# Kernel tuning notes

Hardware: AMD Instinct MI355X
Metric: run time of the kernel (lower is better)

The kernel has to match this reference:

```python
import jax, jax.numpy as jnp
import numpy as np

N, K = 65536, 4
X_SIZE, H_SIZE = 300, 256


def setup_inputs() -> dict:
    key = jax.random.key(0)
    ks = jax.random.split(key, 11)
    s = 0.05  # small init scale for weights
    return {
        "x": jax.random.normal(ks[0], (N, X_SIZE), jnp.float32),
        "h_msgs": jax.random.normal(ks[1], (N, K, H_SIZE), jnp.float32),
        "c_msgs": jax.random.normal(ks[2], (N, K, H_SIZE), jnp.float32),
        "W_iou": jax.random.normal(ks[3], (3 * H_SIZE, X_SIZE), jnp.float32) * s,
        "b_iou": jax.random.normal(ks[4], (3 * H_SIZE,), jnp.float32) * s,
        "U_iou": jax.random.normal(ks[5], (3 * H_SIZE, H_SIZE), jnp.float32) * s,
        "b_Uiou": jax.random.normal(ks[6], (3 * H_SIZE,), jnp.float32) * s,
        "W_f": jax.random.normal(ks[7], (H_SIZE, X_SIZE), jnp.float32) * s,
        "b_Wf": jax.random.normal(ks[8], (H_SIZE,), jnp.float32) * s,
        "U_f": jax.random.normal(ks[9], (H_SIZE, H_SIZE), jnp.float32) * s,
        "b_Uf": jax.random.normal(ks[10], (H_SIZE,), jnp.float32) * s,
    }


def reference(x, h_msgs, c_msgs, W_iou, b_iou, U_iou, b_Uiou, W_f, b_Wf, U_f, b_Uf):
    # ----- reduce_func: gather children states, gated forget sum -----
    h_tild = jnp.sum(h_msgs, axis=1)                              # [N, H]
    wx = (x @ W_f.T + b_Wf)[:, None, :]                           # [N, 1, H]
    uh = jnp.einsum('nkh,gh->nkg', h_msgs, U_f) + b_Uf            # [N, K, H]
    f = jax.nn.sigmoid(wx + uh)                                   # [N, K, H]
    c_tild = jnp.sum(f * c_msgs, axis=1)                          # [N, H]

    # ----- apply_func: fused i/o/u gates -----
    iou = (x @ W_iou.T + b_iou) + (h_tild @ U_iou.T + b_Uiou)     # [N, 3H]
    i, o, u = jnp.split(iou, 3, axis=1)
    i, o, u = jax.nn.sigmoid(i), jax.nn.sigmoid(o), jnp.tanh(u)
    c = i * u + c_tild
    h = o * jnp.tanh(c)
    return jnp.stack((h, c))                                      # [2, N, H]
```

## Files before the change

kernel.cpp:

```cpp
#include <hip/hip_runtime.h>


typedef __attribute__((ext_vector_type(8))) short short8;
typedef __attribute__((ext_vector_type(4))) float f32x4;
typedef __attribute__((ext_vector_type(4))) unsigned short us4;
typedef __attribute__((ext_vector_type(4))) unsigned int u32x4;

#define NN 65536

__device__ __forceinline__ unsigned short f2bf(float f) {
  unsigned int u = __float_as_uint(f);
  u += 0x7FFFu + ((u >> 16) & 1u);
  return (unsigned short)(u >> 16);
}
__device__ __forceinline__ float bf2f(unsigned short s) {
  return __uint_as_float(((unsigned int)s) << 16);
}
__device__ __forceinline__ f32x4 mfma16(short8 a, short8 b, f32x4 c) {
  return __builtin_amdgcn_mfma_f32_16x16x32_bf16(a, b, c, 0, 0, 0);
}
__device__ __forceinline__ float sigmoidf_(float v) { return 1.0f / (1.0f + __expf(-v)); }
__device__ __forceinline__ float ftanh(float v) { return 1.0f - 2.0f / (__expf(2.0f * v) + 1.0f); }

__global__ void prep_all(const float* __restrict__ Wf, const float* __restrict__ Uf,
                         const float* __restrict__ Wiou, const float* __restrict__ Uiou,
                         unsigned short* __restrict__ ws) {
  int idx = blockIdx.x * 256 + threadIdx.x;
  if (idx < 81920) {
    int j = idx & 7, lane = (idx >> 3) & 63, ct = (idx >> 9) & 15, kt = idx >> 13;
    int k = kt*32 + ((lane >> 4) << 3) + j, col = ct*16 + (lane & 15);
    ws[idx] = f2bf(k < 300 ? Wf[col*300 + k] : 0.0f);
  } else if (idx < 147456) {
    int i = idx - 81920;
    int j = i & 7, lane = (i >> 3) & 63, ct = (i >> 9) & 15, kt = i >> 13;
    int k = kt*32 + ((lane >> 4) << 3) + j, col = ct*16 + (lane & 15);
    ws[idx] = f2bf(Uf[col*256 + k]);
  } else {
    int i = idx - 147456;
    int j = i & 7, lane = (i >> 3) & 63;
    int rest = i >> 9, ct = rest % 48, kt = rest / 48;
    int k = kt*32 + ((lane >> 4) << 3) + j;
    int g = (ct % 3)*256 + (ct/3)*16 + (lane & 15);
    float v = (k < 320) ? (k < 300 ? Wiou[g*300 + k] : 0.0f) : Uiou[g*256 + (k - 320)];
    ws[idx] = f2bf(v);
  }
}

__global__ __launch_bounds__(512, 4) void fused_cell(
    const float* __restrict__ x, const float* __restrict__ h_msgs,
    const float* __restrict__ c_msgs,
    const float* __restrict__ b_iou, const float* __restrict__ b_Uiou,
    const float* __restrict__ bWf, const float* __restrict__ bUf,
    const unsigned short* __restrict__ Bwf, const unsigned short* __restrict__ Buf,
    const unsigned short* __restrict__ Biou,
    float* __restrict__ out_h, float* __restrict__ out_c) {
  __shared__ alignas(16) char smem[71168];
  unsigned short* Axh = (unsigned short*)smem;
  unsigned short* Hm  = (unsigned short*)(smem + 37376);
  unsigned short* wfs = (unsigned short*)(smem + 54272);
  unsigned int*   IUO = (unsigned int*)(smem + 37376);

  const int tid = threadIdx.x;
  const int n0 = blockIdx.x * 32;
  const int wave = tid >> 6, lane = tid & 63;
  const int lrow = lane & 15, lgrp = lane >> 4;
  const int nl = wave;
  const f32x4 fz = {0.0f, 0.0f, 0.0f, 0.0f};

  f32x4 hvN[4];

  auto issue_h = [&](int chunk) {
    int node = n0 + chunk*8 + nl;
    const float* hp = h_msgs + (size_t)node*1024 + lane*4;
#pragma unroll
    for (int k = 0; k < 4; ++k) hvN[k] = *(const f32x4*)(hp + k*256);
  };

  auto write_h = [&](int chunk) {
    f32x4 s = fz;
#pragma unroll
    for (int k = 0; k < 4; ++k) {
      us4 o;
#pragma unroll
      for (int e = 0; e < 4; ++e) { s[e] += hvN[k][e]; o[e] = f2bf(hvN[k][e]); }
      *(us4*)&Hm[(nl*4 + k)*264 + lane*4] = o;
    }
    us4 ht;
#pragma unroll
    for (int e = 0; e < 4; ++e) ht[e] = f2bf(s[e]);
    *(us4*)&Axh[(chunk*8 + nl)*584 + 320 + lane*4] = ht;
  };

  auto uh_gemm = [&](f32x4 a2[2][2]) {
    const unsigned short* bp = Buf + ((wave*2)*64 + lane)*8;
    short8 b0 = *(const short8*)bp;
    short8 b1 = *(const short8*)(bp + 512);
#pragma unroll
    for (int ks = 0; ks < 8; ++ks) {
      short8 nb0 = b0, nb1 = b1;
      if (ks < 7) {
        const unsigned short* np = Buf + (((ks+1)*16 + wave*2)*64 + lane)*8;
        nb0 = *(const short8*)np;
        nb1 = *(const short8*)(np + 512);
      }
#pragma unroll
      for (int rt = 0; rt < 2; ++rt) {
        short8 a = *(const short8*)&Hm[(rt*16 + lrow)*264 + ks*32 + lgrp*8];
        a2[rt][0] = mfma16(a, b0, a2[rt][0]);
        a2[rt][1] = mfma16(a, b1, a2[rt][1]);
      }
      b0 = nb0; b1 = nb1;
    }
  };

  issue_h(0);
  for (int i = tid; i < 32*80; i += 512) {
    int r = i / 80, c4 = i - r*80;
    f32x4 v = fz;
    if (c4 < 75) v = *(const f32x4*)&x[(size_t)(n0 + r)*300 + c4*4];
    us4 o;
#pragma unroll
    for (int e = 0; e < 4; ++e) o[e] = f2bf(v[e]);
    *(us4*)&Axh[r*584 + c4*4] = o;
  }
  write_h(0);
  issue_h(1);
  __syncthreads();

  {
    const unsigned short* bp = Bwf + ((wave*2)*64 + lane)*8;
    short8 b0 = *(const short8*)bp;
    short8 b1 = *(const short8*)(bp + 512);
    f32x4 w00 = fz, w01 = fz, w10 = fz, w11 = fz;
#pragma unroll
    for (int ks = 0; ks < 10; ++ks) {
      short8 nb0 = b0, nb1 = b1;
      if (ks < 9) {
        const unsigned short* np = Bwf + (((ks+1)*16 + wave*2)*64 + lane)*8;
        nb0 = *(const short8*)np;
        nb1 = *(const short8*)(np + 512);
      }
      short8 a0 = *(const short8*)&Axh[lrow*584 + ks*32 + lgrp*8];
      short8 a1 = *(const short8*)&Axh[(16 + lrow)*584 + ks*32 + lgrp*8];
      w00 = mfma16(a0, b0, w00); w10 = mfma16(a1, b0, w10);
      w01 = mfma16(a0, b1, w01); w11 = mfma16(a1, b1, w11);
      b0 = nb0; b1 = nb1;
    }
#pragma unroll
    for (int ct = 0; ct < 2; ++ct) {
      int col = wave*32 + ct*16 + lrow;
      float bias = bWf[col];
      f32x4 v0 = ct ? w01 : w00, v1 = ct ? w11 : w10;
#pragma unroll
      for (int r = 0; r < 4; ++r) {
        wfs[(lgrp*4 + r)*264 + col]      = f2bf(v0[r] + bias);
        wfs[(16 + lgrp*4 + r)*264 + col] = f2bf(v1[r] + bias);
      }
    }
  }
  __syncthreads();

  float bu[2];
  bu[0] = bUf[wave*32 + lrow];
  bu[1] = bUf[wave*32 + 16 + lrow];

#pragma unroll
  for (int chunk = 0; chunk < 4; ++chunk) {
    float cm[2][2][4];
#pragma unroll
    for (int rt = 0; rt < 2; ++rt) {
      const float* cp = c_msgs + (size_t)(n0 + chunk*8 + rt*4 + lgrp)*1024 + wave*32 + lrow;
#pragma unroll
      for (int ct2 = 0; ct2 < 2; ++ct2)
#pragma unroll
        for (int r = 0; r < 4; ++r) cm[rt][ct2][r] = cp[r*256 + ct2*16];
    }

    f32x4 a2[2][2] = {{fz, fz}, {fz, fz}};
    uh_gemm(a2);

#pragma unroll
    for (int rt = 0; rt < 2; ++rt) {
      int node = chunk*8 + rt*4 + lgrp;
#pragma unroll
      for (int ct2 = 0; ct2 < 2; ++ct2) {
        int col = wave*32 + ct2*16 + lrow;
        float wfv = bf2f(wfs[node*264 + col]);
        float s = 0.0f;
#pragma unroll
        for (int r = 0; r < 4; ++r) {
          float fg = sigmoidf_(a2[rt][ct2][r] + wfv + bu[ct2]);
          s += fg * cm[rt][ct2][r];
        }
        out_c[(size_t)(n0 + node)*256 + col] = s;
      }
    }
    __syncthreads();
    if (chunk < 3) {
      write_h(chunk + 1);
      if (chunk < 2) issue_h(chunk + 2);
      __syncthreads();
    }
  }

#pragma unroll 1
  for (int p = 0; p < 2; ++p) {
    int cb = wave*2 + p;
    int ct0 = cb*3;
    int col = cb*16 + lrow;
    f32x4 aI0 = fz, aO0 = fz, aU0 = fz, aI1 = fz, aO1 = fz, aU1 = fz;
    const unsigned short* bp = Biou + ((size_t)ct0*64 + lane)*8;
    short8 bi = *(const short8*)bp;
    short8 bo = *(const short8*)(bp + 512);
    short8 bu8 = *(const short8*)(bp + 1024);
#pragma unroll
    for (int ks = 0; ks < 18; ++ks) {
      short8 ni = bi, no = bo, nu = bu8;
      if (ks < 17) {
        const unsigned short* np = Biou + ((size_t)((ks+1)*48 + ct0)*64 + lane)*8;
        ni = *(const short8*)np;
        no = *(const short8*)(np + 512);
        nu = *(const short8*)(np + 1024);
      }
      short8 a0 = *(const short8*)&Axh[lrow*584 + ks*32 + lgrp*8];
      short8 a1 = *(const short8*)&Axh[(16 + lrow)*584 + ks*32 + lgrp*8];
      aI0 = mfma16(a0, bi, aI0);  aI1 = mfma16(a1, bi, aI1);
      aO0 = mfma16(a0, bo, aO0);  aO1 = mfma16(a1, bo, aO1);
      aU0 = mfma16(a0, bu8, aU0); aU1 = mfma16(a1, bu8, aU1);
      bi = ni; bo = no; bu8 = nu;
    }
    float bI = b_iou[col]       + b_Uiou[col];
    float bO = b_iou[256 + col] + b_Uiou[256 + col];
    float bU = b_iou[512 + col] + b_Uiou[512 + col];
#pragma unroll
    for (int rt = 0; rt < 2; ++rt) {
      f32x4 ai = rt ? aI1 : aI0, ao = rt ? aO1 : aO0, au = rt ? aU1 : aU0;
#pragma unroll
      for (int r = 0; r < 4; ++r) {
        float iv = sigmoidf_(ai[r] + bI);
        float ov = sigmoidf_(ao[r] + bO);
        float uv = ftanh(au[r] + bU);
        IUO[(rt*16 + lgrp*4 + r)*260 + col] =
            (unsigned int)f2bf(iv * uv) | ((unsigned int)f2bf(ov) << 16);
      }
    }
  }
  __syncthreads();

#pragma unroll
  for (int chunk = 0; chunk < 4; ++chunk) {
    int nb = chunk*8 + nl;
    size_t base = (size_t)(n0 + nb)*256 + lane*4;
    u32x4 pk = *(const u32x4*)&IUO[nb*260 + lane*4];
    f32x4 ctl = *(const f32x4*)&out_c[base];
    f32x4 hv, cvo;
#pragma unroll
    for (int e = 0; e < 4; ++e) {
      float iu = bf2f((unsigned short)(pk[e] & 0xFFFFu));
      float ov = bf2f((unsigned short)(pk[e] >> 16));
      float c  = iu + ctl[e];
      cvo[e] = c;
      hv[e] = ov * ftanh(c);
    }
    *(f32x4*)&out_h[base] = hv;
    *(f32x4*)&out_c[base] = cvo;
  }
}

extern "C" void kernel_launch(void* const* d_in, const int* in_sizes, int n_in,
                              void* d_out, int out_size, void* d_ws, size_t ws_size,
                              hipStream_t stream) {
  const float* x      = (const float*)d_in[0];
  const float* h_msgs = (const float*)d_in[1];
  const float* c_msgs = (const float*)d_in[2];
  const float* W_iou  = (const float*)d_in[3];
  const float* b_iou  = (const float*)d_in[4];
  const float* U_iou  = (const float*)d_in[5];
  const float* b_Uiou = (const float*)d_in[6];
  const float* W_f    = (const float*)d_in[7];
  const float* b_Wf   = (const float*)d_in[8];
  const float* U_f    = (const float*)d_in[9];
  const float* b_Uf   = (const float*)d_in[10];

  unsigned short* ws   = (unsigned short*)d_ws;
  unsigned short* Bwf  = ws;
  unsigned short* Buf  = ws + 81920;
  unsigned short* Biou = ws + 147456;

  float* h_slot = (float*)d_out;
  float* c_slot = h_slot + (size_t)NN*256;

  prep_all<<<2304, 256, 0, stream>>>(W_f, U_f, W_iou, U_iou, ws);
  fused_cell<<<NN/32, 512, 0, stream>>>(x, h_msgs, c_msgs, b_iou, b_Uiou,
                                        b_Wf, b_Uf, Bwf, Buf, Biou, h_slot, c_slot);
}
```

Baseline: 268.1 us.

## Load h_msgs A-operands directly from global, drop Hm staging and shrink LDS

The U_f GEMM now builds its A operands straight from global h_msgs, converting to packed bf16 in registers with a perm-based pack, instead of staging per-child h in an LDS buffer with barriers around every chunk. This removes the Hm buffer and most per-chunk synchronisation, cutting LDS from about 71KB to 54KB, which may let more blocks fit per CU. The GEMM loops are unrolled two k-steps at a time with deeper B prefetch. The IOU epilogue is split into two half-passes using a smaller packed buffer. The cost is that h_msgs is read from global twice, and the new pack rounds without ties-to-even.

```diff
diff --git a/kernel.cpp b/kernel.cpp
--- a/kernel.cpp
+++ b/kernel.cpp
@@ -15,6 +15,11 @@
 }
 __device__ __forceinline__ float bf2f(unsigned short s) {
   return __uint_as_float(((unsigned int)s) << 16);
+}
+__device__ __forceinline__ unsigned int pkbf(float lo, float hi) {
+  unsigned int a = __float_as_uint(lo) + 0x8000u;
+  unsigned int b = __float_as_uint(hi) + 0x8000u;
+  return __builtin_amdgcn_perm(b, a, 0x07060302u);
 }
 __device__ __forceinline__ f32x4 mfma16(short8 a, short8 b, f32x4 c) {
   return __builtin_amdgcn_mfma_f32_16x16x32_bf16(a, b, c, 0, 0, 0);
@@ -54,11 +59,10 @@
     const unsigned short* __restrict__ Bwf, const unsigned short* __restrict__ Buf,
     const unsigned short* __restrict__ Biou,
     float* __restrict__ out_h, float* __restrict__ out_c) {
-  __shared__ alignas(16) char smem[71168];
+  __shared__ alignas(16) char smem[54272];
   unsigned short* Axh = (unsigned short*)smem;
-  unsigned short* Hm  = (unsigned short*)(smem + 37376);
-  unsigned short* wfs = (unsigned short*)(smem + 54272);
-  unsigned int*   IUO = (unsigned int*)(smem + 37376);
+  unsigned short* wfs = (unsigned short*)(smem + 37376);
+  unsigned int*   IUOp = (unsigned int*)(smem + 37376);
 
   const int tid = threadIdx.x;
   const int n0 = blockIdx.x * 32;
@@ -67,53 +71,14 @@
   const int nl = wave;
   const f32x4 fz = {0.0f, 0.0f, 0.0f, 0.0f};
 
-  f32x4 hvN[4];
-
-  auto issue_h = [&](int chunk) {
-    int node = n0 + chunk*8 + nl;
-    const float* hp = h_msgs + (size_t)node*1024 + lane*4;
-#pragma unroll
-    for (int k = 0; k < 4; ++k) hvN[k] = *(const f32x4*)(hp + k*256);
+  auto ldA = [&](const float* base, int ks) -> short8 {
+    f32x4 v0 = *(const f32x4*)(base + ks*32);
+    f32x4 v1 = *(const f32x4*)(base + ks*32 + 4);
+    u32x4 u = { pkbf(v0[0], v0[1]), pkbf(v0[2], v0[3]),
+                pkbf(v1[0], v1[1]), pkbf(v1[2], v1[3]) };
+    return __builtin_bit_cast(short8, u);
   };
 
-  auto write_h = [&](int chunk) {
-    f32x4 s = fz;
-#pragma unroll
-    for (int k = 0; k < 4; ++k) {
-      us4 o;
-#pragma unroll
-      for (int e = 0; e < 4; ++e) { s[e] += hvN[k][e]; o[e] = f2bf(hvN[k][e]); }
-      *(us4*)&Hm[(nl*4 + k)*264 + lane*4] = o;
-    }
-    us4 ht;
-#pragma unroll
-    for (int e = 0; e < 4; ++e) ht[e] = f2bf(s[e]);
-    *(us4*)&Axh[(chunk*8 + nl)*584 + 320 + lane*4] = ht;
-  };
-
-  auto uh_gemm = [&](f32x4 a2[2][2]) {
-    const unsigned short* bp = Buf + ((wave*2)*64 + lane)*8;
-    short8 b0 = *(const short8*)bp;
-    short8 b1 = *(const short8*)(bp + 512);
-#pragma unroll
-    for (int ks = 0; ks < 8; ++ks) {
-      short8 nb0 = b0, nb1 = b1;
-      if (ks < 7) {
-        const unsigned short* np = Buf + (((ks+1)*16 + wave*2)*64 + lane)*8;
-        nb0 = *(const short8*)np;
-        nb1 = *(const short8*)(np + 512);
-      }
-#pragma unroll
-      for (int rt = 0; rt < 2; ++rt) {
-        short8 a = *(const short8*)&Hm[(rt*16 + lrow)*264 + ks*32 + lgrp*8];
-        a2[rt][0] = mfma16(a, b0, a2[rt][0]);
-        a2[rt][1] = mfma16(a, b1, a2[rt][1]);
-      }
-      b0 = nb0; b1 = nb1;
-    }
-  };
-
-  issue_h(0);
   for (int i = tid; i < 32*80; i += 512) {
     int r = i / 80, c4 = i - r*80;
     f32x4 v = fz;
@@ -123,49 +88,53 @@
     for (int e = 0; e < 4; ++e) o[e] = f2bf(v[e]);
     *(us4*)&Axh[r*584 + c4*4] = o;
   }
-  write_h(0);
-  issue_h(1);
   __syncthreads();
 
   {
-    const unsigned short* bp = Bwf + ((wave*2)*64 + lane)*8;
-    short8 b0 = *(const short8*)bp;
-    short8 b1 = *(const short8*)(bp + 512);
+    const unsigned short* bw = Bwf + (wave*2*64 + lane)*8;
+    short8 c0 = *(const short8*)bw,            c1 = *(const short8*)(bw + 512);
+    short8 d0 = *(const short8*)(bw + 8192),   d1 = *(const short8*)(bw + 8704);
     f32x4 w00 = fz, w01 = fz, w10 = fz, w11 = fz;
 #pragma unroll
-    for (int ks = 0; ks < 10; ++ks) {
-      short8 nb0 = b0, nb1 = b1;
-      if (ks < 9) {
-        const unsigned short* np = Bwf + (((ks+1)*16 + wave*2)*64 + lane)*8;
-        nb0 = *(const short8*)np;
-        nb1 = *(const short8*)(np + 512);
-      }
+    for (int kk = 0; kk < 5; ++kk) {
+      short8 nc0 = c0, nc1 = c1, nd0 = d0, nd1 = d1;
+      if (kk < 4) {
+        const unsigned short* np = bw + (size_t)(kk*2 + 2)*8192;
+        nc0 = *(const short8*)np;          nc1 = *(const short8*)(np + 512);
+        nd0 = *(const short8*)(np + 8192); nd1 = *(const short8*)(np + 8704);
+      }
+      int ks = kk*2;
       short8 a0 = *(const short8*)&Axh[lrow*584 + ks*32 + lgrp*8];
       short8 a1 = *(const short8*)&Axh[(16 + lrow)*584 + ks*32 + lgrp*8];
-      w00 = mfma16(a0, b0, w00); w10 = mfma16(a1, b0, w10);
-      w01 = mfma16(a0, b1, w01); w11 = mfma16(a1, b1, w11);
-      b0 = nb0; b1 = nb1;
-    }
-#pragma unroll
-    for (int ct = 0; ct < 2; ++ct) {
-      int col = wave*32 + ct*16 + lrow;
-      float bias = bWf[col];
-      f32x4 v0 = ct ? w01 : w00, v1 = ct ? w11 : w10;
-#pragma unroll
-      for (int r = 0; r < 4; ++r) {
-        wfs[(lgrp*4 + r)*264 + col]      = f2bf(v0[r] + bias);
-        wfs[(16 + lgrp*4 + r)*264 + col] = f2bf(v1[r] + bias);
-      }
-    }
-  }
-  __syncthreads();
-
-  float bu[2];
-  bu[0] = bUf[wave*32 + lrow];
-  bu[1] = bUf[wave*32 + 16 + lrow];
-
-#pragma unroll
+      w00 = mfma16(a0, c0, w00); w10 = mfma16(a1, c0, w10);
+      w01 = mfma16(a0, c1, w01); w11 = mfma16(a1, c1, w11);
+      short8 b0 = *(const short8*)&Axh[lrow*584 + (ks+1)*32 + lgrp*8];
+      short8 b1 = *(const short8*)&Axh[(16 + lrow)*584 + (ks+1)*32 + lgrp*8];
+      w00 = mfma16(b0, d0, w00); w10 = mfma16(b1, d0, w10);
+      w01 = mfma16(b0, d1, w01); w11 = mfma16(b1, d1, w11);
+      c0 = nc0; c1 = nc1; d0 = nd0; d1 = nd1;
+    }
+    float bias0 = bWf[wave*32 + lrow];
+    float bias1 = bWf[wave*32 + 16 + lrow];
+#pragma unroll
+    for (int r = 0; r < 4; ++r) {
+      wfs[(lgrp*4 + r)*264 + wave*32 + lrow]           = f2bf(w00[r] + bias0);
+      wfs[(lgrp*4 + r)*264 + wave*32 + 16 + lrow]      = f2bf(w01[r] + bias1);
+      wfs[(16 + lgrp*4 + r)*264 + wave*32 + lrow]      = f2bf(w10[r] + bias0);
+      wfs[(16 + lgrp*4 + r)*264 + wave*32 + 16 + lrow] = f2bf(w11[r] + bias1);
+    }
+  }
+
+  const float bu0 = bUf[wave*32 + lrow];
+  const float bu1 = bUf[wave*32 + 16 + lrow];
+
+#pragma unroll 1
   for (int chunk = 0; chunk < 4; ++chunk) {
+    const float* hp = h_msgs + (size_t)(n0 + chunk*8 + nl)*1024 + lane*4;
+    f32x4 t0 = *(const f32x4*)hp;
+    f32x4 t1 = *(const f32x4*)(hp + 256);
+    f32x4 t2 = *(const f32x4*)(hp + 512);
+    f32x4 t3 = *(const f32x4*)(hp + 768);
     float cm[2][2][4];
 #pragma unroll
     for (int rt = 0; rt < 2; ++rt) {
@@ -176,58 +145,91 @@
         for (int r = 0; r < 4; ++r) cm[rt][ct2][r] = cp[r*256 + ct2*16];
     }
 
-    f32x4 a2[2][2] = {{fz, fz}, {fz, fz}};
-    uh_gemm(a2);
+    const float* hA0 = h_msgs + ((size_t)(n0 + chunk*8 + (lrow >> 2))*4 + (lrow & 3))*256 + lgrp*8;
+    const float* hA1 = h_msgs + ((size_t)(n0 + chunk*8 + 4 + (lrow >> 2))*4 + (lrow & 3))*256 + lgrp*8;
+    f32x4 a00 = fz, a01 = fz, a10 = fz, a11 = fz;
+    const unsigned short* bB = Buf + (wave*2*64 + lane)*8;
+    short8 c0 = *(const short8*)bB,          c1 = *(const short8*)(bB + 512);
+    short8 d0 = *(const short8*)(bB + 8192), d1 = *(const short8*)(bB + 8704);
+#pragma unroll
+    for (int kk = 0; kk < 4; ++kk) {
+      short8 nc0 = c0, nc1 = c1, nd0 = d0, nd1 = d1;
+      if (kk < 3) {
+        const unsigned short* np = bB + (size_t)(kk*2 + 2)*8192;
+        nc0 = *(const short8*)np;          nc1 = *(const short8*)(np + 512);
+        nd0 = *(const short8*)(np + 8192); nd1 = *(const short8*)(np + 8704);
+      }
+      int ks = kk*2;
+      short8 A0 = ldA(hA0, ks),   A1 = ldA(hA1, ks);
+      a00 = mfma16(A0, c0, a00);  a01 = mfma16(A0, c1, a01);
+      a10 = mfma16(A1, c0, a10);  a11 = mfma16(A1, c1, a11);
+      short8 B0 = ldA(hA0, ks+1), B1 = ldA(hA1, ks+1);
+      a00 = mfma16(B0, d0, a00);  a01 = mfma16(B0, d1, a01);
+      a10 = mfma16(B1, d0, a10);  a11 = mfma16(B1, d1, a11);
+      c0 = nc0; c1 = nc1; d0 = nd0; d1 = nd1;
+    }
+
+    {
+      us4 ht;
+#pragma unroll
+      for (int e = 0; e < 4; ++e) ht[e] = f2bf(t0[e] + t1[e] + t2[e] + t3[e]);
+      *(us4*)&Axh[(chunk*8 + nl)*584 + 320 + lane*4] = ht;
+    }
 
 #pragma unroll
     for (int rt = 0; rt < 2; ++rt) {
       int node = chunk*8 + rt*4 + lgrp;
+      const f32x4 u0 = rt ? a10 : a00;
+      const f32x4 u1 = rt ? a11 : a01;
 #pragma unroll
       for (int ct2 = 0; ct2 < 2; ++ct2) {
+        const f32x4 uv = ct2 ? u1 : u0;
         int col = wave*32 + ct2*16 + lrow;
         float wfv = bf2f(wfs[node*264 + col]);
+        float bus = ct2 ? bu1 : bu0;
         float s = 0.0f;
 #pragma unroll
-        for (int r = 0; r < 4; ++r) {
-          float fg = sigmoidf_(a2[rt][ct2][r] + wfv + bu[ct2]);
-          s += fg * cm[rt][ct2][r];
-        }
+        for (int r = 0; r < 4; ++r)
+          s += sigmoidf_(uv[r] + wfv + bus) * cm[rt][ct2][r];
         out_c[(size_t)(n0 + node)*256 + col] = s;
       }
     }
-    __syncthreads();
-    if (chunk < 3) {
-      write_h(chunk + 1);
-      if (chunk < 2) issue_h(chunk + 2);
-      __syncthreads();
-    }
-  }
+  }
+  __syncthreads();
 
 #pragma unroll 1
   for (int p = 0; p < 2; ++p) {
-    int cb = wave*2 + p;
-    int ct0 = cb*3;
+    int cb = p*8 + wave;
     int col = cb*16 + lrow;
+    const unsigned short* bi = Biou + ((size_t)(cb*3)*64 + lane)*8;
+    short8 g0 = *(const short8*)bi;
+    short8 g1 = *(const short8*)(bi + 512);
+    short8 g2 = *(const short8*)(bi + 1024);
+    short8 k0 = *(const short8*)(bi + 24576);
+    short8 k1 = *(const short8*)(bi + 25088);
+    short8 k2 = *(const short8*)(bi + 25600);
     f32x4 aI0 = fz, aO0 = fz, aU0 = fz, aI1 = fz, aO1 = fz, aU1 = fz;
-    const unsigned short* bp = Biou + ((size_t)ct0*64 + lane)*8;
-    short8 bi = *(const short8*)bp;
-    short8 bo = *(const short8*)(bp + 512);
-    short8 bu8 = *(const short8*)(bp + 1024);
-#pragma unroll
-    for (int ks = 0; ks < 18; ++ks) {
-      short8 ni = bi, no = bo, nu = bu8;
-      if (ks < 17) {
-        const unsigned short* np = Biou + ((size_t)((ks+1)*48 + ct0)*64 + lane)*8;
-        ni = *(const short8*)np;
-        no = *(const short8*)(np + 512);
-        nu = *(const short8*)(np + 1024);
-      }
-      short8 a0 = *(const short8*)&Axh[lrow*584 + ks*32 + lgrp*8];
-      short8 a1 = *(const short8*)&Axh[(16 + lrow)*584 + ks*32 + lgrp*8];
-      aI0 = mfma16(a0, bi, aI0);  aI1 = mfma16(a1, bi, aI1);
-      aO0 = mfma16(a0, bo, aO0);  aO1 = mfma16(a1, bo, aO1);
-      aU0 = mfma16(a0, bu8, aU0); aU1 = mfma16(a1, bu8, aU1);
-      bi = ni; bo = no; bu8 = nu;
+#pragma unroll
+    for (int kk = 0; kk < 9; ++kk) {
+      short8 n0b = g0, n1b = g1, n2b = g2, m0b = k0, m1b = k1, m2b = k2;
+      if (kk < 8) {
+        const unsigned short* np = bi + (size_t)(kk*2 + 2)*24576;
+        n0b = *(const short8*)np;           n1b = *(const short8*)(np + 512);
+        n2b = *(const short8*)(np + 1024);  m0b = *(const short8*)(np + 24576);
+        m1b = *(const short8*)(np + 25088); m2b = *(const short8*)(np + 25600);
+      }
+      int ks = kk*2;
+      short8 A0 = *(const short8*)&Axh[lrow*584 + ks*32 + lgrp*8];
+      short8 A1 = *(const short8*)&Axh[(16 + lrow)*584 + ks*32 + lgrp*8];
+      aI0 = mfma16(A0, g0, aI0); aI1 = mfma16(A1, g0, aI1);
+      aO0 = mfma16(A0, g1, aO0); aO1 = mfma16(A1, g1, aO1);
+      aU0 = mfma16(A0, g2, aU0); aU1 = mfma16(A1, g2, aU1);
+      short8 B0 = *(const short8*)&Axh[lrow*584 + (ks+1)*32 + lgrp*8];
+      short8 B1 = *(const short8*)&Axh[(16 + lrow)*584 + (ks+1)*32 + lgrp*8];
+      aI0 = mfma16(B0, k0, aI0); aI1 = mfma16(B1, k0, aI1);
+      aO0 = mfma16(B0, k1, aO0); aO1 = mfma16(B1, k1, aO1);
+      aU0 = mfma16(B0, k2, aU0); aU1 = mfma16(B1, k2, aU1);
+      g0 = n0b; g1 = n1b; g2 = n2b; k0 = m0b; k1 = m1b; k2 = m2b;
     }
     float bI = b_iou[col]       + b_Uiou[col];
     float bO = b_iou[256 + col] + b_Uiou[256 + col];
@@ -240,30 +242,28 @@
         float iv = sigmoidf_(ai[r] + bI);
         float ov = sigmoidf_(ao[r] + bO);
         float uv = ftanh(au[r] + bU);
-        IUO[(rt*16 + lgrp*4 + r)*260 + col] =
+        IUOp[(rt*16 + lgrp*4 + r)*132 + wave*16 + lrow] =
             (unsigned int)f2bf(iv * uv) | ((unsigned int)f2bf(ov) << 16);
       }
     }
-  }
-  __syncthreads();
-
-#pragma unroll
-  for (int chunk = 0; chunk < 4; ++chunk) {
-    int nb = chunk*8 + nl;
-    size_t base = (size_t)(n0 + nb)*256 + lane*4;
-    u32x4 pk = *(const u32x4*)&IUO[nb*260 + lane*4];
-    f32x4 ctl = *(const f32x4*)&out_c[base];
-    f32x4 hv, cvo;
-#pragma unroll
-    for (int e = 0; e < 4; ++e) {
-      float iu = bf2f((unsigned short)(pk[e] & 0xFFFFu));
-      float ov = bf2f((unsigned short)(pk[e] >> 16));
-      float c  = iu + ctl[e];
-      cvo[e] = c;
-      hv[e] = ov * ftanh(c);
-    }
-    *(f32x4*)&out_h[base] = hv;
-    *(f32x4*)&out_c[base] = cvo;
+    __syncthreads();
+
+#pragma unroll
+    for (int chunkE = 0; chunkE < 4; ++chunkE) {
+      int nb = chunkE*8 + nl;
+#pragma unroll
+      for (int half = 0; half < 2; ++half) {
+        int slot = half*64 + lane;
+        unsigned int pk = IUOp[nb*132 + slot];
+        size_t base = (size_t)(n0 + nb)*256 + p*128 + slot;
+        float iu = bf2f((unsigned short)(pk & 0xFFFFu));
+        float ov = bf2f((unsigned short)(pk >> 16));
+        float c  = iu + out_c[base];
+        out_c[base] = c;
+        out_h[base] = ov * ftanh(c);
+      }
+    }
+    if (p == 0) __syncthreads();
   }
 }
 
```

After: 501.2 us. 86.9% more time.

## Swizzle LDS layouts, spill Wf result to global, split IOU epilogue by halves

Applied to the files above, without the earlier changes.

Replaces the padded shared-memory row strides with XOR-swizzled layouts for the x/h-tilde and child-h tiles. The W_f·x result is parked in out_h in fp32 instead of in a bf16 LDS buffer. The IOU gate buffer is halved by processing column halves per pass with an interleaved epilogue. Together these cut LDS footprint (71KB to 53KB) so more blocks can be resident, at the cost of extra global round-trips through out_h and an additional barrier.

```diff
diff --git a/kernel.cpp b/kernel.cpp
--- a/kernel.cpp
+++ b/kernel.cpp
@@ -4,7 +4,6 @@
 typedef __attribute__((ext_vector_type(8))) short short8;
 typedef __attribute__((ext_vector_type(4))) float f32x4;
 typedef __attribute__((ext_vector_type(4))) unsigned short us4;
-typedef __attribute__((ext_vector_type(4))) unsigned int u32x4;
 
 #define NN 65536
 
@@ -54,11 +53,8 @@
     const unsigned short* __restrict__ Bwf, const unsigned short* __restrict__ Buf,
     const unsigned short* __restrict__ Biou,
     float* __restrict__ out_h, float* __restrict__ out_c) {
-  __shared__ alignas(16) char smem[71168];
-  unsigned short* Axh = (unsigned short*)smem;
-  unsigned short* Hm  = (unsigned short*)(smem + 37376);
-  unsigned short* wfs = (unsigned short*)(smem + 54272);
-  unsigned int*   IUO = (unsigned int*)(smem + 37376);
+  __shared__ alignas(16) char smem[53248];
+  unsigned int* IUOp = (unsigned int*)(smem + 36864);
 
   const int tid = threadIdx.x;
   const int n0 = blockIdx.x * 32;
@@ -67,6 +63,13 @@
   const int nl = wave;
   const f32x4 fz = {0.0f, 0.0f, 0.0f, 0.0f};
 
+  auto axp = [&](int row, int colB) -> char* {
+    return smem + ((row*1152 + colB) ^ ((row & 7) << 4));
+  };
+  auto hmp = [&](int row, int colB) -> char* {
+    return smem + 36864 + ((row*512 + colB) ^ ((row & 7) << 4));
+  };
+
   f32x4 hvN[4];
 
   auto issue_h = [&](int chunk) {
@@ -83,12 +86,12 @@
       us4 o;
 #pragma unroll
       for (int e = 0; e < 4; ++e) { s[e] += hvN[k][e]; o[e] = f2bf(hvN[k][e]); }
-      *(us4*)&Hm[(nl*4 + k)*264 + lane*4] = o;
+      *(us4*)hmp(nl*4 + k, lane*8) = o;
     }
     us4 ht;
 #pragma unroll
     for (int e = 0; e < 4; ++e) ht[e] = f2bf(s[e]);
-    *(us4*)&Axh[(chunk*8 + nl)*584 + 320 + lane*4] = ht;
+    *(us4*)axp(chunk*8 + nl, 640 + lane*8) = ht;
   };
 
   auto uh_gemm = [&](f32x4 a2[2][2]) {
@@ -105,7 +108,7 @@
       }
 #pragma unroll
       for (int rt = 0; rt < 2; ++rt) {
-        short8 a = *(const short8*)&Hm[(rt*16 + lrow)*264 + ks*32 + lgrp*8];
+        short8 a = *(const short8*)hmp(rt*16 + lrow, ks*64 + lgrp*16);
         a2[rt][0] = mfma16(a, b0, a2[rt][0]);
         a2[rt][1] = mfma16(a, b1, a2[rt][1]);
       }
@@ -121,7 +124,7 @@
     us4 o;
 #pragma unroll
     for (int e = 0; e < 4; ++e) o[e] = f2bf(v[e]);
-    *(us4*)&Axh[r*584 + c4*4] = o;
+    *(us4*)axp(r, c4*8) = o;
   }
   write_h(0);
   issue_h(1);
@@ -140,8 +143,8 @@
         nb0 = *(const short8*)np;
         nb1 = *(const short8*)(np + 512);
       }
-      short8 a0 = *(const short8*)&Axh[lrow*584 + ks*32 + lgrp*8];
-      short8 a1 = *(const short8*)&Axh[(16 + lrow)*584 + ks*32 + lgrp*8];
+      short8 a0 = *(const short8*)axp(lrow, ks*64 + lgrp*16);
+      short8 a1 = *(const short8*)axp(16 + lrow, ks*64 + lgrp*16);
       w00 = mfma16(a0, b0, w00); w10 = mfma16(a1, b0, w10);
       w01 = mfma16(a0, b1, w01); w11 = mfma16(a1, b1, w11);
       b0 = nb0; b1 = nb1;
@@ -153,8 +156,8 @@
       f32x4 v0 = ct ? w01 : w00, v1 = ct ? w11 : w10;
 #pragma unroll
       for (int r = 0; r < 4; ++r) {
-        wfs[(lgrp*4 + r)*264 + col]      = f2bf(v0[r] + bias);
-        wfs[(16 + lgrp*4 + r)*264 + col] = f2bf(v1[r] + bias);
+        out_h[(size_t)(n0 + lgrp*4 + r)*256 + col]      = v0[r] + bias;
+        out_h[(size_t)(n0 + 16 + lgrp*4 + r)*256 + col] = v1[r] + bias;
       }
     }
   }
@@ -167,13 +170,17 @@
 #pragma unroll
   for (int chunk = 0; chunk < 4; ++chunk) {
     float cm[2][2][4];
+    float wfv[2][2];
 #pragma unroll
     for (int rt = 0; rt < 2; ++rt) {
-      const float* cp = c_msgs + (size_t)(n0 + chunk*8 + rt*4 + lgrp)*1024 + wave*32 + lrow;
-#pragma unroll
-      for (int ct2 = 0; ct2 < 2; ++ct2)
+      int node = chunk*8 + rt*4 + lgrp;
+      const float* cp = c_msgs + (size_t)(n0 + node)*1024 + wave*32 + lrow;
+#pragma unroll
+      for (int ct2 = 0; ct2 < 2; ++ct2) {
+        wfv[rt][ct2] = out_h[(size_t)(n0 + node)*256 + wave*32 + ct2*16 + lrow];
 #pragma unroll
         for (int r = 0; r < 4; ++r) cm[rt][ct2][r] = cp[r*256 + ct2*16];
+      }
     }
 
     f32x4 a2[2][2] = {{fz, fz}, {fz, fz}};
@@ -185,11 +192,10 @@
 #pragma unroll
       for (int ct2 = 0; ct2 < 2; ++ct2) {
         int col = wave*32 + ct2*16 + lrow;
-        float wfv = bf2f(wfs[node*264 + col]);
         float s = 0.0f;
 #pragma unroll
         for (int r = 0; r < 4; ++r) {
-          float fg = sigmoidf_(a2[rt][ct2][r] + wfv + bu[ct2]);
+          float fg = sigmoidf_(a2[rt][ct2][r] + wfv[rt][ct2] + bu[ct2]);
           s += fg * cm[rt][ct2][r];
         }
         out_c[(size_t)(n0 + node)*256 + col] = s;
@@ -205,7 +211,7 @@
 
 #pragma unroll 1
   for (int p = 0; p < 2; ++p) {
-    int cb = wave*2 + p;
+    int cb = p*8 + wave;
     int ct0 = cb*3;
     int col = cb*16 + lrow;
     f32x4 aI0 = fz, aO0 = fz, aU0 = fz, aI1 = fz, aO1 = fz, aU1 = fz;
@@ -222,8 +228,8 @@
         no = *(const short8*)(np + 512);
         nu = *(const short8*)(np + 1024);
       }
-      short8 a0 = *(const short8*)&Axh[lrow*584 + ks*32 + lgrp*8];
-      short8 a1 = *(const short8*)&Axh[(16 + lrow)*584 + ks*32 + lgrp*8];
+      short8 a0 = *(const short8*)axp(lrow, ks*64 + lgrp*16);
+      short8 a1 = *(const short8*)axp(16 + lrow, ks*64 + lgrp*16);
       aI0 = mfma16(a0, bi, aI0);  aI1 = mfma16(a1, bi, aI1);
       aO0 = mfma16(a0, bo, aO0);  aO1 = mfma16(a1, bo, aO1);
       aU0 = mfma16(a0, bu8, aU0); aU1 = mfma16(a1, bu8, aU1);
@@ -240,30 +246,25 @@
         float iv = sigmoidf_(ai[r] + bI);
         float ov = sigmoidf_(ao[r] + bO);
         float uv = ftanh(au[r] + bU);
-        IUO[(rt*16 + lgrp*4 + r)*260 + col] =
+        IUOp[(rt*16 + lgrp*4 + r)*128 + wave*16 + lrow] =
             (unsigned int)f2bf(iv * uv) | ((unsigned int)f2bf(ov) << 16);
       }
     }
-  }
-  __syncthreads();
-
-#pragma unroll
-  for (int chunk = 0; chunk < 4; ++chunk) {
-    int nb = chunk*8 + nl;
-    size_t base = (size_t)(n0 + nb)*256 + lane*4;
-    u32x4 pk = *(const u32x4*)&IUO[nb*260 + lane*4];
-    f32x4 ctl = *(const f32x4*)&out_c[base];
-    f32x4 hv, cvo;
-#pragma unroll
-    for (int e = 0; e < 4; ++e) {
-      float iu = bf2f((unsigned short)(pk[e] & 0xFFFFu));
-      float ov = bf2f((unsigned short)(pk[e] >> 16));
-      float c  = iu + ctl[e];
-      cvo[e] = c;
-      hv[e] = ov * ftanh(c);
-    }
-    *(f32x4*)&out_h[base] = hv;
-    *(f32x4*)&out_c[base] = cvo;
+    __syncthreads();
+
+#pragma unroll
+    for (int e = 0; e < 8; ++e) {
+      int idx = e*512 + tid;
+      int node = idx >> 7, slot = idx & 127;
+      unsigned int pk = IUOp[node*128 + slot];
+      size_t base = (size_t)(n0 + node)*256 + p*128 + slot;
+      float iu = bf2f((unsigned short)(pk & 0xFFFFu));
+      float ov = bf2f((unsigned short)(pk >> 16));
+      float c  = iu + out_c[base];
+      out_c[base] = c;
+      out_h[base] = ov * ftanh(c);
+    }
+    if (p == 0) __syncthreads();
   }
 }
 
```

Measured after the change: 312.7 us. +16.6%, slower.
